# Optimization experiments

Hardware: AMD Instinct MI355X
Metric: run time of the kernel (lower is better)

The kernel has to match this reference:

```python
import jax, jax.numpy as jnp
import numpy as np

N_NODES = 50000
N_EDGES = 800000
NFEAT = 128
NHID = 128
BN_EPS = 1e-5


def setup_inputs() -> dict:
    key = jax.random.key(0)
    ks = jax.random.split(key, 8)
    x = jax.random.normal(ks[0], (N_NODES, NFEAT), dtype=jnp.float32)
    edge_index = jax.random.randint(ks[1], (2, N_EDGES), 0, N_NODES, dtype=jnp.int64)
    # Linear weights in torch layout [out, in]; scaled like kaiming-ish init.
    W1 = jax.random.normal(ks[2], (NHID, NFEAT), dtype=jnp.float32) / np.sqrt(NFEAT)
    b1 = jax.random.normal(ks[3], (NHID,), dtype=jnp.float32) * 0.01
    gamma = jnp.ones((NHID,), dtype=jnp.float32)
    beta = jnp.zeros((NHID,), dtype=jnp.float32)
    W2 = jax.random.normal(ks[4], (NHID, NHID), dtype=jnp.float32) / np.sqrt(NHID)
    b2 = jax.random.normal(ks[5], (NHID,), dtype=jnp.float32) * 0.01
    return {"x": x, "edge_index": edge_index, "W1": W1, "b1": b1,
            "gamma": gamma, "beta": beta, "W2": W2, "b2": b2}


def reference(x, edge_index, W1, b1, gamma, beta, W2, b2):
    # GINConv, eps = 0: h = (1 + eps) * x + sum_{j in N(i)} x_j
    src, dst = edge_index[0], edge_index[1]
    agg = x + jax.ops.segment_sum(x[src], dst, num_segments=N_NODES)  # [N, nfeat]
    # MLP: Linear -> ReLU -> BatchNorm1d (training stats) -> Linear
    h = jnp.maximum(agg @ W1.T + b1, 0.0)                             # [N, nhid]
    mean = jnp.mean(h, axis=0)
    var = jnp.var(h, axis=0)  # biased variance, as torch BN uses for normalization
    h = (h - mean) * jax.lax.rsqrt(var + BN_EPS) * gamma + beta
    return h @ W2.T + b2
```

## Files before the change

kernel.cpp:

```cpp
#include <hip/hip_runtime.h>

#define N_NODES 50000
#define N_EDGES 800000
#define NF 128
#define BN_EPS 1e-5f
#define G_ROWS 32
#define GBLOCKS ((N_NODES + G_ROWS - 1) / G_ROWS)
#define NB 1568
#define SCAN_BLOCKS ((N_NODES + 255) / 256)
#define AP 136
#define HP 132

typedef __attribute__((ext_vector_type(8))) short short8;
typedef __attribute__((ext_vector_type(4))) float f32x4;

__device__ __forceinline__ unsigned short f2bf(float f) {
    union { float f; unsigned int i; } v; v.f = f;
    unsigned int r = (v.i + 0x7fffu + ((v.i >> 16) & 1u)) >> 16;
    return (unsigned short)r;
}
__device__ __forceinline__ float bf2f(unsigned short u) {
    union { unsigned int i; float f; } v; v.i = ((unsigned int)u) << 16; return v.f;
}
__device__ __forceinline__ float bflo(unsigned int u) { return bf2f((unsigned short)(u & 0xffffu)); }
__device__ __forceinline__ float bfhi(unsigned int u) { return bf2f((unsigned short)(u >> 16)); }

#define SETUP_C (N_NODES * NF / 4)
#define SETUP_P (128 * 128)
__global__ void setup_kernel(const float* __restrict__ x, unsigned short* __restrict__ xb,
                             const float* __restrict__ W1, const float* __restrict__ W2,
                             unsigned short* __restrict__ Wb1, unsigned short* __restrict__ Wb2,
                             int* __restrict__ counts, float* __restrict__ stats,
                             int do_convert) {
    int i = blockIdx.x * blockDim.x + threadIdx.x;
    int off = do_convert ? 0 : SETUP_C;
    i += off;
    if (i < SETUP_C) {
        float4 v = ((const float4*)x)[i];
        ushort4 u;
        u.x = f2bf(v.x); u.y = f2bf(v.y); u.z = f2bf(v.z); u.w = f2bf(v.w);
        ((ushort4*)xb)[i] = u;
    } else if (i < SETUP_C + SETUP_P) {
        int j = i - SETUP_C;
        Wb1[j] = f2bf(W1[j]);
        Wb2[j] = f2bf(W2[j]);
    } else if (i < SETUP_C + SETUP_P + N_NODES) {
        counts[i - SETUP_C - SETUP_P] = 0;
    } else if (i < SETUP_C + SETUP_P + N_NODES + 256) {
        stats[i - SETUP_C - SETUP_P - N_NODES] = 0.0f;
    }
}

__global__ void hist_kernel(const int* __restrict__ ei, int* __restrict__ counts,
                            int* __restrict__ rank) {
    int t = blockIdx.x * blockDim.x + threadIdx.x;
    if (t < N_EDGES) rank[t] = atomicAdd(&counts[ei[N_EDGES + t]], 1);
}

__global__ __launch_bounds__(256) void scan_reduce(const int* __restrict__ counts,
                                                   int* __restrict__ partials) {
    __shared__ int red[256];
    int t = threadIdx.x;
    int i = blockIdx.x * 256 + t;
    red[t] = (i < N_NODES) ? counts[i] : 0;
    __syncthreads();
    for (int off = 128; off > 0; off >>= 1) {
        if (t < off) red[t] += red[t + off];
        __syncthreads();
    }
    if (t == 0) partials[blockIdx.x] = red[0];
}

__global__ __launch_bounds__(256) void scan_apply(const int* __restrict__ counts,
                                                  const int* __restrict__ partials,
                                                  int* __restrict__ rowptr) {
    __shared__ int sp[256];
    __shared__ int s[256];
    int t = threadIdx.x;

    int pv = (t < SCAN_BLOCKS) ? partials[t] : 0;
    sp[t] = pv;
    __syncthreads();
    for (int off = 1; off < 256; off <<= 1) {
        int u = (t >= off) ? sp[t - off] : 0;
        __syncthreads();
        sp[t] += u;
        __syncthreads();
    }
    int blockOff = (blockIdx.x == 0) ? 0 : sp[blockIdx.x - 1];

    int i = blockIdx.x * 256 + t;
    int v = (i < N_NODES) ? counts[i] : 0;
    s[t] = v;
    __syncthreads();
    for (int off = 1; off < 256; off <<= 1) {
        int u = (t >= off) ? s[t - off] : 0;
        __syncthreads();
        s[t] += u;
        __syncthreads();
    }
    int excl = blockOff + s[t] - v;
    if (i < N_NODES) rowptr[i] = excl;
    if (i == 0) rowptr[N_NODES] = N_EDGES;
}

__global__ void fill_kernel(const int* __restrict__ ei,
                            const int* __restrict__ rowptr,
                            const int* __restrict__ rank,
                            int* __restrict__ ssrc) {
    int t = blockIdx.x * blockDim.x + threadIdx.x;
    if (t < N_EDGES) {
        int dst = ei[N_EDGES + t];
        ssrc[rowptr[dst] + rank[t]] = ei[t];
    }
}

__global__ __launch_bounds__(256, 6) void fused_gather_gemm1_bf16(
    const unsigned short* __restrict__ xb,
    const int* __restrict__ rowptr,
    const int* __restrict__ ssrc,
    const unsigned short* __restrict__ Wb,
    const float* __restrict__ b1,
    unsigned short* __restrict__ buf,
    float* __restrict__ P) {
    __shared__ __align__(16) char smem[G_ROWS * HP * 4];
    unsigned short (*At)[AP] = (unsigned short (*)[AP])smem;
    float (*Ht)[HP] = (float (*)[HP])smem;

    int t = threadIdx.x;
    int wave = t >> 6, lane = t & 63;
    int base = blockIdx.x * G_ROWS;
    int nrows = N_NODES - base; if (nrows > G_ROWS) nrows = G_ROWS;

    const unsigned int* x2 = (const unsigned int*)xb;

    for (int nn = 0; nn < 8; nn++) {
        int r = wave * 8 + nn;
        int node = base + r;
        unsigned int packed = 0u;
        if (node < N_NODES) {
            unsigned int u = x2[(size_t)node * 64 + lane];
            float ax = bflo(u), ay = bfhi(u);
            int beg = rowptr[node], end = rowptr[node + 1];
            int e = beg;
            for (; e + 15 < end; e += 16) {
                unsigned int uu[16];
#pragma unroll
                for (int k = 0; k < 16; k++) uu[k] = x2[(size_t)ssrc[e + k] * 64 + lane];
#pragma unroll
                for (int k = 0; k < 16; k++) { ax += bflo(uu[k]); ay += bfhi(uu[k]); }
            }
            for (; e + 3 < end; e += 4) {
                unsigned int u0 = x2[(size_t)ssrc[e] * 64 + lane];
                unsigned int u1 = x2[(size_t)ssrc[e + 1] * 64 + lane];
                unsigned int u2 = x2[(size_t)ssrc[e + 2] * 64 + lane];
                unsigned int u3 = x2[(size_t)ssrc[e + 3] * 64 + lane];
                ax += bflo(u0) + bflo(u1) + bflo(u2) + bflo(u3);
                ay += bfhi(u0) + bfhi(u1) + bfhi(u2) + bfhi(u3);
            }
            for (; e < end; e++) {
                unsigned int u0 = x2[(size_t)ssrc[e] * 64 + lane];
                ax += bflo(u0);
                ay += bfhi(u0);
            }
            packed = ((unsigned int)f2bf(ay) << 16) | (unsigned int)f2bf(ax);
        }
        ((unsigned int*)&At[r][0])[lane] = packed;
    }
    __syncthreads();

    int m0 = (wave & 1) * 16;
    int n0 = (wave >> 1) * 64;
    int l15 = lane & 15, q = lane >> 4;

    f32x4 acc[4];
#pragma unroll
    for (int i = 0; i < 4; i++) acc[i] = (f32x4){0.f, 0.f, 0.f, 0.f};

#pragma unroll
    for (int kc = 0; kc < 4; kc++) {
        short8 a = *((const short8*)&At[m0 + l15][kc * 32 + q * 8]);
#pragma unroll
        for (int tile = 0; tile < 4; tile++) {
            short8 b = *((const short8*)(Wb + (size_t)(n0 + 16 * tile + l15) * 128 + kc * 32 + q * 8));
            acc[tile] = __builtin_amdgcn_mfma_f32_16x16x32_bf16(a, b, acc[tile], 0, 0, 0);
        }
    }
    __syncthreads();

#pragma unroll
    for (int tile = 0; tile < 4; tile++) {
        int col = n0 + 16 * tile + l15;
        float bias = b1[col];
#pragma unroll
        for (int reg = 0; reg < 4; reg++) {
            int row = q * 4 + reg;
            Ht[m0 + row][col] = fmaxf(acc[tile][reg] + bias, 0.f);
        }
    }
    __syncthreads();

    for (int i = t; i < G_ROWS * 32; i += 256) {
        int r = i >> 5, c4 = i & 31;
        int row = base + r;
        if (row < N_NODES) {
            float4 v = *((const float4*)&Ht[r][c4 * 4]);
            ushort4 u;
            u.x = f2bf(v.x); u.y = f2bf(v.y); u.z = f2bf(v.z); u.w = f2bf(v.w);
            *((ushort4*)(buf + (size_t)row * NF + c4 * 4)) = u;
        }
    }

    {
        int f = t & 127;
        bool issq = (t >= 128);
        float s = 0.f;
        for (int r = 0; r < nrows; r++) {
            float v = Ht[r][f];
            s += issq ? v * v : v;
        }
        P[(size_t)t * NB + blockIdx.x] = s;
    }
}

__global__ __launch_bounds__(256) void bn_reduce(const float* __restrict__ P,
                                                 const float* __restrict__ gamma,
                                                 const float* __restrict__ beta,
                                                 float* __restrict__ ab) {
    __shared__ float s1[256], s2[256];
    int f = blockIdx.x;
    int j = threadIdx.x;
    float a = 0.f, b = 0.f;
    for (int k = j; k < GBLOCKS; k += 256) {
        a += P[(size_t)f * NB + k];
        b += P[(size_t)(128 + f) * NB + k];
    }
    s1[j] = a; s2[j] = b;
    __syncthreads();
    for (int off = 128; off > 0; off >>= 1) {
        if (j < off) { s1[j] += s1[j + off]; s2[j] += s2[j + off]; }
        __syncthreads();
    }
    if (j == 0) {
        float mean = s1[0] * (1.0f / N_NODES);
        float var = s2[0] * (1.0f / N_NODES) - mean * mean;
        float rstd = rsqrtf(var + BN_EPS);
        float aa = gamma[f] * rstd;
        float cc = beta[f] - mean * aa;
        ab[f] = aa;
        ab[128 + f] = cc;
    }
}

__global__ __launch_bounds__(256) void gemm2_bf16(
    const unsigned short* __restrict__ buf,
    const unsigned short* __restrict__ Wb,
    const float* __restrict__ b2,
    const float* __restrict__ ab,
    float* __restrict__ out) {
    __shared__ __align__(16) char smem[G_ROWS * HP * 4];
    unsigned short (*At)[AP] = (unsigned short (*)[AP])smem;
    float (*Ht)[HP] = (float (*)[HP])smem;

    int t = threadIdx.x;
    int base = blockIdx.x * G_ROWS;
    int nrows = N_NODES - base; if (nrows > G_ROWS) nrows = G_ROWS;

    for (int i = t; i < G_ROWS * 32; i += 256) {
        int r = i >> 5, c4 = i & 31;
        ushort4 u = make_ushort4(0, 0, 0, 0);
        if (r < nrows) {
            ushort4 hv = *((const ushort4*)(buf + (size_t)(base + r) * NF + c4 * 4));
            float4 av = ((const float4*)ab)[c4];
            float4 cv = ((const float4*)(ab + 128))[c4];
            u.x = f2bf(bf2f(hv.x) * av.x + cv.x);
            u.y = f2bf(bf2f(hv.y) * av.y + cv.y);
            u.z = f2bf(bf2f(hv.z) * av.z + cv.z);
            u.w = f2bf(bf2f(hv.w) * av.w + cv.w);
        }
        *((ushort4*)&At[r][c4 * 4]) = u;
    }
    __syncthreads();

    int wave = t >> 6, lane = t & 63;
    int m0 = (wave & 1) * 16;
    int n0 = (wave >> 1) * 64;
    int l15 = lane & 15, q = lane >> 4;

    f32x4 acc[4];
#pragma unroll
    for (int i = 0; i < 4; i++) acc[i] = (f32x4){0.f, 0.f, 0.f, 0.f};

#pragma unroll
    for (int kc = 0; kc < 4; kc++) {
        short8 a = *((const short8*)&At[m0 + l15][kc * 32 + q * 8]);
#pragma unroll
        for (int tile = 0; tile < 4; tile++) {
            short8 b = *((const short8*)(Wb + (size_t)(n0 + 16 * tile + l15) * 128 + kc * 32 + q * 8));
            acc[tile] = __builtin_amdgcn_mfma_f32_16x16x32_bf16(a, b, acc[tile], 0, 0, 0);
        }
    }
    __syncthreads();

#pragma unroll
    for (int tile = 0; tile < 4; tile++) {
        int col = n0 + 16 * tile + l15;
        float bias = b2[col];
#pragma unroll
        for (int reg = 0; reg < 4; reg++) {
            int row = q * 4 + reg;
            Ht[m0 + row][col] = acc[tile][reg] + bias;
        }
    }
    __syncthreads();

    for (int i = t; i < G_ROWS * 32; i += 256) {
        int r = i >> 5, c4 = i & 31;
        int row = base + r;
        if (row < N_NODES)
            *((float4*)(out + (size_t)row * NF + c4 * 4)) = *((const float4*)&Ht[r][c4 * 4]);
    }
}

__global__ void finalize_bn(const float* __restrict__ stats,
                            const float* __restrict__ gamma,
                            const float* __restrict__ beta,
                            float* __restrict__ ab) {
    int f = threadIdx.x;
    if (f < 128) {
        float mean = stats[f] * (1.0f / N_NODES);
        float var = stats[128 + f] * (1.0f / N_NODES) - mean * mean;
        float rstd = rsqrtf(var + BN_EPS);
        float a = gamma[f] * rstd;
        float c = beta[f] - mean * a;
        ab[f] = a;
        ab[128 + f] = c;
    }
}

__global__ __launch_bounds__(256) void fused_gather_gemm1_f32(
    const float* __restrict__ xv,
    const int* __restrict__ rowptr,
    const int* __restrict__ ssrc,
    const unsigned short* __restrict__ Wb,
    const float* __restrict__ b1,
    float* __restrict__ hout,
    float* __restrict__ stats) {
    __shared__ unsigned short At[G_ROWS][AP];
    __shared__ float Ht[G_ROWS][HP];

    int t = threadIdx.x;
    int wave = t >> 6, lane = t & 63;
    int base = blockIdx.x * G_ROWS;
    int nrows = N_NODES - base; if (nrows > G_ROWS) nrows = G_ROWS;

    const float2* xf2 = (const float2*)xv;

    for (int nn = 0; nn < 8; nn++) {
        int r = wave * 8 + nn;
        int node = base + r;
        float2 acc = make_float2(0.f, 0.f);
        if (node < N_NODES) {
            acc = xf2[(size_t)node * 64 + lane];
            int beg = rowptr[node], end = rowptr[node + 1];
            for (int e = beg; e < end; e++) {
                float2 v0 = xf2[(size_t)ssrc[e] * 64 + lane];
                acc.x += v0.x;
                acc.y += v0.y;
            }
        }
        unsigned int packed = ((unsigned int)f2bf(acc.y) << 16) | (unsigned int)f2bf(acc.x);
        *((unsigned int*)&At[r][lane * 2]) = packed;
    }
    __syncthreads();

    int m0 = (wave & 1) * 16;
    int n0 = (wave >> 1) * 64;
    int l15 = lane & 15, q = lane >> 4;

    f32x4 acc[4];
#pragma unroll
    for (int i = 0; i < 4; i++) acc[i] = (f32x4){0.f, 0.f, 0.f, 0.f};

#pragma unroll
    for (int kc = 0; kc < 4; kc++) {
        short8 a = *((const short8*)&At[m0 + l15][kc * 32 + q * 8]);
#pragma unroll
        for (int tile = 0; tile < 4; tile++) {
            short8 b = *((const short8*)(Wb + (size_t)(n0 + 16 * tile + l15) * 128 + kc * 32 + q * 8));
            acc[tile] = __builtin_amdgcn_mfma_f32_16x16x32_bf16(a, b, acc[tile], 0, 0, 0);
        }
    }

#pragma unroll
    for (int tile = 0; tile < 4; tile++) {
        int col = n0 + 16 * tile + l15;
        float bias = b1[col];
#pragma unroll
        for (int reg = 0; reg < 4; reg++) {
            int row = q * 4 + reg;
            Ht[m0 + row][col] = fmaxf(acc[tile][reg] + bias, 0.f);
        }
    }
    __syncthreads();

    for (int i = t; i < G_ROWS * 32; i += 256) {
        int r = i >> 5, c4 = i & 31;
        int row = base + r;
        if (row < N_NODES)
            *((float4*)(hout + (size_t)row * NF + c4 * 4)) = *((const float4*)&Ht[r][c4 * 4]);
    }

    if (t < 128) {
        float s = 0.f, sq = 0.f;
        for (int r = 0; r < nrows; r++) {
            float v = Ht[r][t];
            s += v; sq += v * v;
        }
        atomicAdd(&stats[t], s);
        atomicAdd(&stats[128 + t], sq);
    }
}

__global__ __launch_bounds__(256) void gemm2_f32(
    float* __restrict__ h,
    const unsigned short* __restrict__ Wb,
    const float* __restrict__ b2,
    const float* __restrict__ ab) {
    __shared__ unsigned short At[G_ROWS][AP];
    __shared__ float Ht[G_ROWS][HP];

    int t = threadIdx.x;
    int base = blockIdx.x * G_ROWS;
    int nrows = N_NODES - base; if (nrows > G_ROWS) nrows = G_ROWS;

    for (int i = t; i < G_ROWS * 32; i += 256) {
        int r = i >> 5, c4 = i & 31;
        float4 v = make_float4(0.f, 0.f, 0.f, 0.f);
        if (r < nrows) {
            float4 hv = ((const float4*)(h + (size_t)(base + r) * NF))[c4];
            float4 av = ((const float4*)ab)[c4];
            float4 cv = ((const float4*)(ab + 128))[c4];
            v.x = hv.x * av.x + cv.x;
            v.y = hv.y * av.y + cv.y;
            v.z = hv.z * av.z + cv.z;
            v.w = hv.w * av.w + cv.w;
        }
        ushort4 u;
        u.x = f2bf(v.x); u.y = f2bf(v.y); u.z = f2bf(v.z); u.w = f2bf(v.w);
        *((ushort4*)&At[r][c4 * 4]) = u;
    }
    __syncthreads();

    int wave = t >> 6, lane = t & 63;
    int m0 = (wave & 1) * 16;
    int n0 = (wave >> 1) * 64;
    int l15 = lane & 15, q = lane >> 4;

    f32x4 acc[4];
#pragma unroll
    for (int i = 0; i < 4; i++) acc[i] = (f32x4){0.f, 0.f, 0.f, 0.f};

#pragma unroll
    for (int kc = 0; kc < 4; kc++) {
        short8 a = *((const short8*)&At[m0 + l15][kc * 32 + q * 8]);
#pragma unroll
        for (int tile = 0; tile < 4; tile++) {
            short8 b = *((const short8*)(Wb + (size_t)(n0 + 16 * tile + l15) * 128 + kc * 32 + q * 8));
            acc[tile] = __builtin_amdgcn_mfma_f32_16x16x32_bf16(a, b, acc[tile], 0, 0, 0);
        }
    }

#pragma unroll
    for (int tile = 0; tile < 4; tile++) {
        int col = n0 + 16 * tile + l15;
        float bias = b2[col];
#pragma unroll
        for (int reg = 0; reg < 4; reg++) {
            int row = q * 4 + reg;
            Ht[m0 + row][col] = acc[tile][reg] + bias;
        }
    }
    __syncthreads();

    for (int i = t; i < G_ROWS * 32; i += 256) {
        int r = i >> 5, c4 = i & 31;
        int row = base + r;
        if (row < N_NODES)
            *((float4*)(h + (size_t)row * NF + c4 * 4)) = *((const float4*)&Ht[r][c4 * 4]);
    }
}

extern "C" void kernel_launch(void* const* d_in, const int* in_sizes, int n_in,
                              void* d_out, int out_size, void* d_ws, size_t ws_size,
                              hipStream_t stream) {
    const float* x     = (const float*)d_in[0];
    const int*   ei    = (const int*)d_in[1];
    const float* W1    = (const float*)d_in[2];
    const float* b1    = (const float*)d_in[3];
    const float* gamma = (const float*)d_in[4];
    const float* beta  = (const float*)d_in[5];
    const float* W2    = (const float*)d_in[6];
    const float* b2    = (const float*)d_in[7];

    float* out = (float*)d_out;

    float*          stats    = (float*)d_ws;
    float*          ab       = stats + 256;
    float*          P        = ab + 256;
    unsigned short* Wb1      = (unsigned short*)(P + 256 * NB);
    unsigned short* Wb2      = Wb1 + 128 * 128;
    int*            counts   = (int*)(Wb2 + 128 * 128);
    int*            rowptr   = counts + N_NODES;
    int*            partials = rowptr + N_NODES + 1;
    int*            rank     = partials + 256;
    int*            ssrc     = rank + N_EDGES;
    unsigned short* xb       = (unsigned short*)(ssrc + N_EDGES);
    unsigned short* buf      = xb + (size_t)N_NODES * NF;

    size_t need = (size_t)((char*)(buf + (size_t)N_NODES * NF) - (char*)d_ws);
    bool bf16_path = ws_size >= need;

    if (bf16_path) {
        int total = SETUP_C + SETUP_P + N_NODES + 256;
        setup_kernel<<<(total + 255) / 256, 256, 0, stream>>>(
            x, xb, W1, W2, Wb1, Wb2, counts, stats, 1);
    } else {
        int total = SETUP_P + N_NODES + 256;
        setup_kernel<<<(total + 255) / 256, 256, 0, stream>>>(
            x, xb, W1, W2, Wb1, Wb2, counts, stats, 0);
    }
    hist_kernel<<<(N_EDGES + 255) / 256, 256, 0, stream>>>(ei, counts, rank);
    scan_reduce<<<SCAN_BLOCKS, 256, 0, stream>>>(counts, partials);
    scan_apply<<<SCAN_BLOCKS, 256, 0, stream>>>(counts, partials, rowptr);
    fill_kernel<<<(N_EDGES + 255) / 256, 256, 0, stream>>>(ei, rowptr, rank, ssrc);

    if (bf16_path) {
        fused_gather_gemm1_bf16<<<GBLOCKS, 256, 0, stream>>>(
            xb, rowptr, ssrc, Wb1, b1, buf, P);
        bn_reduce<<<128, 256, 0, stream>>>(P, gamma, beta, ab);
        gemm2_bf16<<<GBLOCKS, 256, 0, stream>>>(buf, Wb2, b2, ab, out);
    } else {
        fused_gather_gemm1_f32<<<GBLOCKS, 256, 0, stream>>>(
            x, rowptr, ssrc, Wb1, b1, out, stats);
        finalize_bn<<<1, 128, 0, stream>>>(stats, gamma, beta, ab);
        gemm2_f32<<<GBLOCKS, 256, 0, stream>>>(out, Wb2, b2, ab);
    }
}
```

Baseline: 224.7 us.

## Fuse histogram into setup kernel and double gather block threads

Merges the edge histogram (atomic rank computation) with the bf16 conversion of x and the weights into one launch, and replaces the counts zeroing with a hipMemsetAsync, which removes one kernel launch and lets the atomics overlap with the conversion traffic. The fused gather+GEMM1 kernel now runs 512 threads per block, so each wave gathers 4 rows instead of 8 and covers 32 output columns instead of 64. This gives more waves in flight to hide gather latency, at the cost of higher per-block register and occupancy pressure. The stats zeroing that setup_kernel used to do appears to be dropped on this path, which is harmless only if stats is unused on the bf16 path.

```diff
diff --git a/kernel.cpp b/kernel.cpp
--- a/kernel.cpp
+++ b/kernel.cpp
@@ -27,6 +27,29 @@
 
 #define SETUP_C (N_NODES * NF / 4)
 #define SETUP_P (128 * 128)
+
+#define SH_TOTAL (N_EDGES + SETUP_C + SETUP_P)
+__global__ void setup_hist(const int* __restrict__ ei,
+                           int* __restrict__ counts, int* __restrict__ rank,
+                           const float* __restrict__ x, unsigned short* __restrict__ xb,
+                           const float* __restrict__ W1, const float* __restrict__ W2,
+                           unsigned short* __restrict__ Wb1, unsigned short* __restrict__ Wb2) {
+    int i = blockIdx.x * blockDim.x + threadIdx.x;
+    if (i < N_EDGES) {
+        rank[i] = atomicAdd(&counts[ei[N_EDGES + i]], 1);
+    } else if (i < N_EDGES + SETUP_C) {
+        int j = i - N_EDGES;
+        float4 v = ((const float4*)x)[j];
+        ushort4 u;
+        u.x = f2bf(v.x); u.y = f2bf(v.y); u.z = f2bf(v.z); u.w = f2bf(v.w);
+        ((ushort4*)xb)[j] = u;
+    } else if (i < SH_TOTAL) {
+        int j = i - N_EDGES - SETUP_C;
+        Wb1[j] = f2bf(W1[j]);
+        Wb2[j] = f2bf(W2[j]);
+    }
+}
+
 __global__ void setup_kernel(const float* __restrict__ x, unsigned short* __restrict__ xb,
                              const float* __restrict__ W1, const float* __restrict__ W2,
                              unsigned short* __restrict__ Wb1, unsigned short* __restrict__ Wb2,
@@ -115,7 +138,7 @@
     }
 }
 
-__global__ __launch_bounds__(256, 6) void fused_gather_gemm1_bf16(
+__global__ __launch_bounds__(512, 8) void fused_gather_gemm1_bf16(
     const unsigned short* __restrict__ xb,
     const int* __restrict__ rowptr,
     const int* __restrict__ ssrc,
@@ -134,8 +157,8 @@
 
     const unsigned int* x2 = (const unsigned int*)xb;
 
-    for (int nn = 0; nn < 8; nn++) {
-        int r = wave * 8 + nn;
+    for (int nn = 0; nn < 4; nn++) {
+        int r = wave * 4 + nn;
         int node = base + r;
         unsigned int packed = 0u;
         if (node < N_NODES) {
@@ -170,18 +193,18 @@
     __syncthreads();
 
     int m0 = (wave & 1) * 16;
-    int n0 = (wave >> 1) * 64;
+    int n0 = (wave >> 1) * 32;
     int l15 = lane & 15, q = lane >> 4;
 
-    f32x4 acc[4];
-#pragma unroll
-    for (int i = 0; i < 4; i++) acc[i] = (f32x4){0.f, 0.f, 0.f, 0.f};
+    f32x4 acc[2];
+#pragma unroll
+    for (int i = 0; i < 2; i++) acc[i] = (f32x4){0.f, 0.f, 0.f, 0.f};
 
 #pragma unroll
     for (int kc = 0; kc < 4; kc++) {
         short8 a = *((const short8*)&At[m0 + l15][kc * 32 + q * 8]);
 #pragma unroll
-        for (int tile = 0; tile < 4; tile++) {
+        for (int tile = 0; tile < 2; tile++) {
             short8 b = *((const short8*)(Wb + (size_t)(n0 + 16 * tile + l15) * 128 + kc * 32 + q * 8));
             acc[tile] = __builtin_amdgcn_mfma_f32_16x16x32_bf16(a, b, acc[tile], 0, 0, 0);
         }
@@ -189,7 +212,7 @@
     __syncthreads();
 
 #pragma unroll
-    for (int tile = 0; tile < 4; tile++) {
+    for (int tile = 0; tile < 2; tile++) {
         int col = n0 + 16 * tile + l15;
         float bias = b1[col];
 #pragma unroll
@@ -200,7 +223,7 @@
     }
     __syncthreads();
 
-    for (int i = t; i < G_ROWS * 32; i += 256) {
+    for (int i = t; i < G_ROWS * 32; i += 512) {
         int r = i >> 5, c4 = i & 31;
         int row = base + r;
         if (row < N_NODES) {
@@ -211,7 +234,7 @@
         }
     }
 
-    {
+    if (t < 256) {
         int f = t & 127;
         bool issq = (t >= 128);
         float s = 0.f;
@@ -522,25 +545,24 @@
     bool bf16_path = ws_size >= need;
 
     if (bf16_path) {
-        int total = SETUP_C + SETUP_P + N_NODES + 256;
-        setup_kernel<<<(total + 255) / 256, 256, 0, stream>>>(
-            x, xb, W1, W2, Wb1, Wb2, counts, stats, 1);
+        hipMemsetAsync(counts, 0, N_NODES * sizeof(int), stream);
+        setup_hist<<<(SH_TOTAL + 255) / 256, 256, 0, stream>>>(
+            ei, counts, rank, x, xb, W1, W2, Wb1, Wb2);
+        scan_reduce<<<SCAN_BLOCKS, 256, 0, stream>>>(counts, partials);
+        scan_apply<<<SCAN_BLOCKS, 256, 0, stream>>>(counts, partials, rowptr);
+        fill_kernel<<<(N_EDGES + 255) / 256, 256, 0, stream>>>(ei, rowptr, rank, ssrc);
+        fused_gather_gemm1_bf16<<<GBLOCKS, 512, 0, stream>>>(
+            xb, rowptr, ssrc, Wb1, b1, buf, P);
+        bn_reduce<<<128, 256, 0, stream>>>(P, gamma, beta, ab);
+        gemm2_bf16<<<GBLOCKS, 256, 0, stream>>>(buf, Wb2, b2, ab, out);
     } else {
         int total = SETUP_P + N_NODES + 256;
         setup_kernel<<<(total + 255) / 256, 256, 0, stream>>>(
             x, xb, W1, W2, Wb1, Wb2, counts, stats, 0);
-    }
-    hist_kernel<<<(N_EDGES + 255) / 256, 256, 0, stream>>>(ei, counts, rank);
-    scan_reduce<<<SCAN_BLOCKS, 256, 0, stream>>>(counts, partials);
-    scan_apply<<<SCAN_BLOCKS, 256, 0, stream>>>(counts, partials, rowptr);
-    fill_kernel<<<(N_EDGES + 255) / 256, 256, 0, stream>>>(ei, rowptr, rank, ssrc);
-
-    if (bf16_path) {
-        fused_gather_gemm1_bf16<<<GBLOCKS, 256, 0, stream>>>(
-            xb, rowptr, ssrc, Wb1, b1, buf, P);
-        bn_reduce<<<128, 256, 0, stream>>>(P, gamma, beta, ab);
-        gemm2_bf16<<<GBLOCKS, 256, 0, stream>>>(buf, Wb2, b2, ab, out);
-    } else {
+        hist_kernel<<<(N_EDGES + 255) / 256, 256, 0, stream>>>(ei, counts, rank);
+        scan_reduce<<<SCAN_BLOCKS, 256, 0, stream>>>(counts, partials);
+        scan_apply<<<SCAN_BLOCKS, 256, 0, stream>>>(counts, partials, rowptr);
+        fill_kernel<<<(N_EDGES + 255) / 256, 256, 0, stream>>>(ei, rowptr, rank, ssrc);
         fused_gather_gemm1_f32<<<GBLOCKS, 256, 0, stream>>>(
             x, rowptr, ssrc, Wb1, b1, out, stats);
         finalize_bn<<<1, 128, 0, stream>>>(stats, gamma, beta, ab);
```

New measurement: 224.9 us. Within noise of the previous version (+0.1%).

## Replace CSR build with fixed-capacity per-node buckets plus overflow list

Applied to the files above, without the earlier changes.

Drops the histogram, two-pass scan and fill kernels and instead scatters each edge's source into a fixed 32-slot bucket per destination node using atomic counters. Edges beyond the cap go to a global overflow list that the gather kernel scans linearly for high-degree nodes. The bucket build is fused with the bf16 conversion of x and the weights into one launch, and counters are cleared with a memset. This removes several kernel launches and passes over the edge list, but it costs a larger bucket array and a non-deterministic edge order within each bucket. Overflow past 8192 entries would silently drop edges.

```diff
diff --git a/kernel.cpp b/kernel.cpp
--- a/kernel.cpp
+++ b/kernel.cpp
@@ -7,9 +7,10 @@
 #define G_ROWS 32
 #define GBLOCKS ((N_NODES + G_ROWS - 1) / G_ROWS)
 #define NB 1568
-#define SCAN_BLOCKS ((N_NODES + 255) / 256)
 #define AP 136
 #define HP 132
+#define CAP 32
+#define OVFCAP 8192
 
 typedef __attribute__((ext_vector_type(8))) short short8;
 typedef __attribute__((ext_vector_type(4))) float f32x4;
@@ -27,98 +28,45 @@
 
 #define SETUP_C (N_NODES * NF / 4)
 #define SETUP_P (128 * 128)
-__global__ void setup_kernel(const float* __restrict__ x, unsigned short* __restrict__ xb,
-                             const float* __restrict__ W1, const float* __restrict__ W2,
-                             unsigned short* __restrict__ Wb1, unsigned short* __restrict__ Wb2,
-                             int* __restrict__ counts, float* __restrict__ stats,
-                             int do_convert) {
+
+__global__ void scatter_build(const int* __restrict__ ei,
+                              int* __restrict__ counts, int* __restrict__ ovfcnt,
+                              int* __restrict__ ovf, int* __restrict__ bucket,
+                              const float* __restrict__ x, unsigned short* __restrict__ xb,
+                              const float* __restrict__ W1, const float* __restrict__ W2,
+                              unsigned short* __restrict__ Wb1, unsigned short* __restrict__ Wb2,
+                              int do_convert) {
     int i = blockIdx.x * blockDim.x + threadIdx.x;
-    int off = do_convert ? 0 : SETUP_C;
-    i += off;
-    if (i < SETUP_C) {
-        float4 v = ((const float4*)x)[i];
+    if (!do_convert && i >= N_EDGES) i += SETUP_C;
+    if (i < N_EDGES) {
+        int dst = ei[N_EDGES + i];
+        int src = ei[i];
+        int k = atomicAdd(&counts[dst], 1);
+        if (k < CAP) {
+            bucket[dst * CAP + k] = src;
+        } else {
+            int o = atomicAdd(ovfcnt, 1);
+            if (o < OVFCAP) { ovf[2 * o] = dst; ovf[2 * o + 1] = src; }
+        }
+    } else if (i < N_EDGES + SETUP_C) {
+        int j = i - N_EDGES;
+        float4 v = ((const float4*)x)[j];
         ushort4 u;
         u.x = f2bf(v.x); u.y = f2bf(v.y); u.z = f2bf(v.z); u.w = f2bf(v.w);
-        ((ushort4*)xb)[i] = u;
-    } else if (i < SETUP_C + SETUP_P) {
-        int j = i - SETUP_C;
+        ((ushort4*)xb)[j] = u;
+    } else if (i < N_EDGES + SETUP_C + SETUP_P) {
+        int j = i - N_EDGES - SETUP_C;
         Wb1[j] = f2bf(W1[j]);
         Wb2[j] = f2bf(W2[j]);
-    } else if (i < SETUP_C + SETUP_P + N_NODES) {
-        counts[i - SETUP_C - SETUP_P] = 0;
-    } else if (i < SETUP_C + SETUP_P + N_NODES + 256) {
-        stats[i - SETUP_C - SETUP_P - N_NODES] = 0.0f;
-    }
-}
-
-__global__ void hist_kernel(const int* __restrict__ ei, int* __restrict__ counts,
-                            int* __restrict__ rank) {
-    int t = blockIdx.x * blockDim.x + threadIdx.x;
-    if (t < N_EDGES) rank[t] = atomicAdd(&counts[ei[N_EDGES + t]], 1);
-}
-
-__global__ __launch_bounds__(256) void scan_reduce(const int* __restrict__ counts,
-                                                   int* __restrict__ partials) {
-    __shared__ int red[256];
-    int t = threadIdx.x;
-    int i = blockIdx.x * 256 + t;
-    red[t] = (i < N_NODES) ? counts[i] : 0;
-    __syncthreads();
-    for (int off = 128; off > 0; off >>= 1) {
-        if (t < off) red[t] += red[t + off];
-        __syncthreads();
-    }
-    if (t == 0) partials[blockIdx.x] = red[0];
-}
-
-__global__ __launch_bounds__(256) void scan_apply(const int* __restrict__ counts,
-                                                  const int* __restrict__ partials,
-                                                  int* __restrict__ rowptr) {
-    __shared__ int sp[256];
-    __shared__ int s[256];
-    int t = threadIdx.x;
-
-    int pv = (t < SCAN_BLOCKS) ? partials[t] : 0;
-    sp[t] = pv;
-    __syncthreads();
-    for (int off = 1; off < 256; off <<= 1) {
-        int u = (t >= off) ? sp[t - off] : 0;
-        __syncthreads();
-        sp[t] += u;
-        __syncthreads();
-    }
-    int blockOff = (blockIdx.x == 0) ? 0 : sp[blockIdx.x - 1];
-
-    int i = blockIdx.x * 256 + t;
-    int v = (i < N_NODES) ? counts[i] : 0;
-    s[t] = v;
-    __syncthreads();
-    for (int off = 1; off < 256; off <<= 1) {
-        int u = (t >= off) ? s[t - off] : 0;
-        __syncthreads();
-        s[t] += u;
-        __syncthreads();
-    }
-    int excl = blockOff + s[t] - v;
-    if (i < N_NODES) rowptr[i] = excl;
-    if (i == 0) rowptr[N_NODES] = N_EDGES;
-}
-
-__global__ void fill_kernel(const int* __restrict__ ei,
-                            const int* __restrict__ rowptr,
-                            const int* __restrict__ rank,
-                            int* __restrict__ ssrc) {
-    int t = blockIdx.x * blockDim.x + threadIdx.x;
-    if (t < N_EDGES) {
-        int dst = ei[N_EDGES + t];
-        ssrc[rowptr[dst] + rank[t]] = ei[t];
     }
 }
 
 __global__ __launch_bounds__(256, 6) void fused_gather_gemm1_bf16(
     const unsigned short* __restrict__ xb,
-    const int* __restrict__ rowptr,
-    const int* __restrict__ ssrc,
+    const int* __restrict__ counts,
+    const int* __restrict__ bucket,
+    const int* __restrict__ ovfcnt,
+    const int* __restrict__ ovf,
     const unsigned short* __restrict__ Wb,
     const float* __restrict__ b1,
     unsigned short* __restrict__ buf,
@@ -133,6 +81,7 @@
     int nrows = N_NODES - base; if (nrows > G_ROWS) nrows = G_ROWS;
 
     const unsigned int* x2 = (const unsigned int*)xb;
+    int novf = *ovfcnt; if (novf > OVFCAP) novf = OVFCAP;
 
     for (int nn = 0; nn < 8; nn++) {
         int r = wave * 8 + nn;
@@ -141,27 +90,38 @@
         if (node < N_NODES) {
             unsigned int u = x2[(size_t)node * 64 + lane];
             float ax = bflo(u), ay = bfhi(u);
-            int beg = rowptr[node], end = rowptr[node + 1];
-            int e = beg;
-            for (; e + 15 < end; e += 16) {
+            int deg = counts[node];
+            int cnt = deg < CAP ? deg : CAP;
+            const int* bkt = bucket + (size_t)node * CAP;
+            int e = 0;
+            for (; e + 15 < cnt; e += 16) {
                 unsigned int uu[16];
 #pragma unroll
-                for (int k = 0; k < 16; k++) uu[k] = x2[(size_t)ssrc[e + k] * 64 + lane];
+                for (int k = 0; k < 16; k++) uu[k] = x2[(size_t)bkt[e + k] * 64 + lane];
 #pragma unroll
                 for (int k = 0; k < 16; k++) { ax += bflo(uu[k]); ay += bfhi(uu[k]); }
             }
-            for (; e + 3 < end; e += 4) {
-                unsigned int u0 = x2[(size_t)ssrc[e] * 64 + lane];
-                unsigned int u1 = x2[(size_t)ssrc[e + 1] * 64 + lane];
-                unsigned int u2 = x2[(size_t)ssrc[e + 2] * 64 + lane];
-                unsigned int u3 = x2[(size_t)ssrc[e + 3] * 64 + lane];
+            for (; e + 3 < cnt; e += 4) {
+                unsigned int u0 = x2[(size_t)bkt[e] * 64 + lane];
+                unsigned int u1 = x2[(size_t)bkt[e + 1] * 64 + lane];
+                unsigned int u2 = x2[(size_t)bkt[e + 2] * 64 + lane];
+                unsigned int u3 = x2[(size_t)bkt[e + 3] * 64 + lane];
                 ax += bflo(u0) + bflo(u1) + bflo(u2) + bflo(u3);
                 ay += bfhi(u0) + bfhi(u1) + bfhi(u2) + bfhi(u3);
             }
-            for (; e < end; e++) {
-                unsigned int u0 = x2[(size_t)ssrc[e] * 64 + lane];
+            for (; e < cnt; e++) {
+                unsigned int u0 = x2[(size_t)bkt[e] * 64 + lane];
                 ax += bflo(u0);
                 ay += bfhi(u0);
+            }
+            if (deg > CAP) {
+                for (int o = 0; o < novf; o++) {
+                    if (ovf[2 * o] == node) {
+                        unsigned int u0 = x2[(size_t)ovf[2 * o + 1] * 64 + lane];
+                        ax += bflo(u0);
+                        ay += bfhi(u0);
+                    }
+                }
             }
             packed = ((unsigned int)f2bf(ay) << 16) | (unsigned int)f2bf(ax);
         }
@@ -340,8 +300,10 @@
 
 __global__ __launch_bounds__(256) void fused_gather_gemm1_f32(
     const float* __restrict__ xv,
-    const int* __restrict__ rowptr,
-    const int* __restrict__ ssrc,
+    const int* __restrict__ counts,
+    const int* __restrict__ bucket,
+    const int* __restrict__ ovfcnt,
+    const int* __restrict__ ovf,
     const unsigned short* __restrict__ Wb,
     const float* __restrict__ b1,
     float* __restrict__ hout,
@@ -355,6 +317,7 @@
     int nrows = N_NODES - base; if (nrows > G_ROWS) nrows = G_ROWS;
 
     const float2* xf2 = (const float2*)xv;
+    int novf = *ovfcnt; if (novf > OVFCAP) novf = OVFCAP;
 
     for (int nn = 0; nn < 8; nn++) {
         int r = wave * 8 + nn;
@@ -362,11 +325,22 @@
         float2 acc = make_float2(0.f, 0.f);
         if (node < N_NODES) {
             acc = xf2[(size_t)node * 64 + lane];
-            int beg = rowptr[node], end = rowptr[node + 1];
-            for (int e = beg; e < end; e++) {
-                float2 v0 = xf2[(size_t)ssrc[e] * 64 + lane];
+            int deg = counts[node];
+            int cnt = deg < CAP ? deg : CAP;
+            const int* bkt = bucket + (size_t)node * CAP;
+            for (int e = 0; e < cnt; e++) {
+                float2 v0 = xf2[(size_t)bkt[e] * 64 + lane];
                 acc.x += v0.x;
                 acc.y += v0.y;
+            }
+            if (deg > CAP) {
+                for (int o = 0; o < novf; o++) {
+                    if (ovf[2 * o] == node) {
+                        float2 v0 = xf2[(size_t)ovf[2 * o + 1] * 64 + lane];
+                        acc.x += v0.x;
+                        acc.y += v0.y;
+                    }
+                }
             }
         }
         unsigned int packed = ((unsigned int)f2bf(acc.y) << 16) | (unsigned int)f2bf(acc.x);
@@ -511,38 +485,33 @@
     unsigned short* Wb1      = (unsigned short*)(P + 256 * NB);
     unsigned short* Wb2      = Wb1 + 128 * 128;
     int*            counts   = (int*)(Wb2 + 128 * 128);
-    int*            rowptr   = counts + N_NODES;
-    int*            partials = rowptr + N_NODES + 1;
-    int*            rank     = partials + 256;
-    int*            ssrc     = rank + N_EDGES;
-    unsigned short* xb       = (unsigned short*)(ssrc + N_EDGES);
+    int*            ovfcnt   = counts + N_NODES;
+    int*            ovf      = ovfcnt + 16;
+    int*            bucket   = ovf + 2 * OVFCAP;
+    unsigned short* xb       = (unsigned short*)(bucket + (size_t)N_NODES * CAP);
     unsigned short* buf      = xb + (size_t)N_NODES * NF;
 
     size_t need = (size_t)((char*)(buf + (size_t)N_NODES * NF) - (char*)d_ws);
+    size_t need_fb = (size_t)((char*)xb - (char*)d_ws);
     bool bf16_path = ws_size >= need;
 
     if (bf16_path) {
-        int total = SETUP_C + SETUP_P + N_NODES + 256;
-        setup_kernel<<<(total + 255) / 256, 256, 0, stream>>>(
-            x, xb, W1, W2, Wb1, Wb2, counts, stats, 1);
-    } else {
-        int total = SETUP_P + N_NODES + 256;
-        setup_kernel<<<(total + 255) / 256, 256, 0, stream>>>(
-            x, xb, W1, W2, Wb1, Wb2, counts, stats, 0);
-    }
-    hist_kernel<<<(N_EDGES + 255) / 256, 256, 0, stream>>>(ei, counts, rank);
-    scan_reduce<<<SCAN_BLOCKS, 256, 0, stream>>>(counts, partials);
-    scan_apply<<<SCAN_BLOCKS, 256, 0, stream>>>(counts, partials, rowptr);
-    fill_kernel<<<(N_EDGES + 255) / 256, 256, 0, stream>>>(ei, rowptr, rank, ssrc);
-
-    if (bf16_path) {
+        hipMemsetAsync(counts, 0, (N_NODES + 16) * sizeof(int), stream);
+        int total = N_EDGES + SETUP_C + SETUP_P;
+        scatter_build<<<(total + 255) / 256, 256, 0, stream>>>(
+            ei, counts, ovfcnt, ovf, bucket, x, xb, W1, W2, Wb1, Wb2, 1);
         fused_gather_gemm1_bf16<<<GBLOCKS, 256, 0, stream>>>(
-            xb, rowptr, ssrc, Wb1, b1, buf, P);
+            xb, counts, bucket, ovfcnt, ovf, Wb1, b1, buf, P);
         bn_reduce<<<128, 256, 0, stream>>>(P, gamma, beta, ab);
         gemm2_bf16<<<GBLOCKS, 256, 0, stream>>>(buf, Wb2, b2, ab, out);
-    } else {
+    } else if (ws_size >= need_fb) {
+        hipMemsetAsync(counts, 0, (N_NODES + 16) * sizeof(int), stream);
+        hipMemsetAsync(stats, 0, 256 * sizeof(float), stream);
+        int total = N_EDGES + SETUP_P;
+        scatter_build<<<(total + 255) / 256, 256, 0, stream>>>(
+            ei, counts, ovfcnt, ovf, bucket, x, (unsigned short*)0, W1, W2, Wb1, Wb2, 0);
         fused_gather_gemm1_f32<<<GBLOCKS, 256, 0, stream>>>(
-            x, rowptr, ssrc, Wb1, b1, out, stats);
+            x, counts, bucket, ovfcnt, ovf, Wb1, b1, out, stats);
         finalize_bn<<<1, 128, 0, stream>>>(stats, gamma, beta, ab);
         gemm2_f32<<<GBLOCKS, 256, 0, stream>>>(out, Wb2, b2, ab);
     }
```

After: 219.8 us. -2.2%, faster.
